# Optimization experiments

Hardware: AMD Instinct MI355X
Metric: run time of the kernel (lower is better)

## Reference

```python
import jax, jax.numpy as jnp
import numpy as np

B, S, F = 8, 4096, 512
H, A, L, DK = 8, 512, 64, 33  # n_head, n_attn, n_landmarks, d_kernel
D = A // H  # d_k = 64


def setup_inputs() -> dict:
    key = jax.random.key(0)
    ks = jax.random.split(key, 12)
    s = 0.02
    return {
        "query": jax.random.normal(ks[0], (B, S, F), jnp.float32),
        "key": jax.random.normal(ks[1], (B, S, F), jnp.float32),
        "value": jax.random.normal(ks[2], (B, S, F), jnp.float32),
        "mask": jnp.ones((B, 1, S), jnp.bool_),
        "Wq": jax.random.normal(ks[3], (F, A), jnp.float32) * s,
        "bq": jnp.zeros((A,), jnp.float32),
        "Wk": jax.random.normal(ks[4], (F, A), jnp.float32) * s,
        "bk": jnp.zeros((A,), jnp.float32),
        "Wv": jax.random.normal(ks[5], (F, A), jnp.float32) * s,
        "bv": jnp.zeros((A,), jnp.float32),
        "Wo": jax.random.normal(ks[6], (A, F), jnp.float32) * s,
        "bo": jnp.zeros((F,), jnp.float32),
        "conv_w": jax.random.normal(ks[7], (H, 1, DK, 1), jnp.float32) * s,
    }


def iterative_inv(mat, n_iter=6):
    # mat: [B, H, L, L]
    I = jnp.eye(mat.shape[-1], dtype=mat.dtype)
    K = mat
    denom = jnp.max(jnp.sum(K, axis=-2), axis=-1)[:, :, None, None]
    V = jnp.swapaxes(K, -1, -2) / denom
    for _ in range(n_iter):
        KV = K @ V
        V = 0.25 * V @ (13 * I - KV @ (15 * I - KV @ (7 * I - KV)))
    return V


def reference(query, key, value, mask, Wq, bq, Wk, bk, Wv, bv, Wo, bo, conv_w):
    nb, seq, _ = query.shape
    q = (query @ Wq + bq).reshape(nb, seq, H, D).transpose(0, 2, 1, 3)  # [B,H,S,D]
    k = (key @ Wk + bk).reshape(nb, seq, H, D).transpose(0, 2, 1, 3)
    v = (value @ Wv + bv).reshape(nb, seq, H, D).transpose(0, 2, 1, 3)
    scale = D ** -0.25
    q = q * scale
    k = k * scale
    m = seq // L + 1  # segment length per landmark
    q_rep = jnp.concatenate([q, q, q], axis=2)[:, :, : m * L, :]
    k_rep = jnp.concatenate([k, k, k], axis=2)[:, :, : m * L, :]
    q_land = q_rep.reshape(nb, H, L, m, D).mean(axis=3)  # [B,H,L,D]
    k_land = k_rep.reshape(nb, H, L, m, D).mean(axis=3)
    ker1 = jax.nn.softmax(jnp.einsum("bhsd,bhld->bhsl", q, k_land), axis=-1)
    ker2 = jax.nn.softmax(jnp.einsum("bhld,bhmd->bhlm", q_land, k_land), axis=-1)
    ker3 = jax.nn.softmax(jnp.einsum("bhld,bhsd->bhls", q_land, k), axis=-1)
    x = ker1 @ (iterative_inv(ker2) @ (ker3 @ v))  # [B,H,S,D]
    # depthwise conv over the sequence axis (kernel (DK,1), groups=H)
    pad = DK // 2
    conv_out = jax.lax.conv_general_dilated(
        v, conv_w, window_strides=(1, 1), padding=((pad, pad), (0, 0)),
        feature_group_count=H, dimension_numbers=("NCHW", "OIHW", "NCHW"))
    x = x + conv_out
    x = x.transpose(0, 2, 1, 3).reshape(nb, seq, H * D)
    return x @ Wo + bo
```

## Files before the change

### kernel.cpp

```cpp
#include <hip/hip_runtime.h>
#include <hip/hip_bf16.h>
#include <hip/hip_fp16.h>

#define SEQ 4096
#define NBATCH 8
#define NHEAD 8
#define DKW 33
#define LDP 68

typedef _Float16 f16x8 __attribute__((ext_vector_type(8)));
typedef _Float16 f16x4 __attribute__((ext_vector_type(4)));
typedef float f32x4 __attribute__((ext_vector_type(4)));

__global__ __launch_bounds__(256) void cvt_w_k(const float* __restrict__ W, _Float16* __restrict__ Wt, float scale)
{
  __shared__ float T[64][65];
  int n0 = blockIdx.x * 64, k0 = blockIdx.y * 64;
  int tid = threadIdx.x;
#pragma unroll
  for (int i = 0; i < 16; i++) {
    int e = i * 256 + tid; int r = e >> 6, c = e & 63;
    T[r][c] = W[(size_t)(k0 + r) * 512 + n0 + c];
  }
  __syncthreads();
#pragma unroll
  for (int i = 0; i < 16; i++) {
    int e = i * 256 + tid; int r = e >> 6, c = e & 63;
    Wt[(size_t)(n0 + r) * 512 + k0 + c] = (_Float16)(T[c][r] * scale);
  }
}

template<typename TA, int ABHSD, int OUTL>
__global__ __launch_bounds__(256) void gemm_f16_k(
    const TA* __restrict__ A, const _Float16* __restrict__ Wt,
    const float* __restrict__ bias, float bscale, void* __restrict__ outp)
{
  __shared__ _Float16 Al[2][128 * 40];
  __shared__ _Float16 Bl[2][128 * 40];
  const int tid = threadIdx.x;
  const int lane = tid & 63, wave = tid >> 6;
  const int wr = wave >> 1, wc = wave & 1;
  const int row0 = blockIdx.x * 128, col0 = blockIdx.y * 128;
  const int ar = tid >> 2;
  const int ak = (tid & 3) * 8;
  const int grA0 = row0 + ar, grA1 = row0 + ar + 64;
  size_t bsA0, bsA1;
  if constexpr (ABHSD) {
    bsA0 = ((size_t)(grA0 >> 12) * NHEAD * SEQ + (grA0 & 4095)) * 64;
    bsA1 = ((size_t)(grA1 >> 12) * NHEAD * SEQ + (grA1 & 4095)) * 64;
  } else {
    bsA0 = (size_t)grA0 * 512;
    bsA1 = (size_t)grA1 * 512;
  }
  const size_t bsB0 = (size_t)(col0 + ar) * 512, bsB1 = (size_t)(col0 + ar + 64) * 512;
  const int lA0 = ar * 40 + ak, lA1 = (ar + 64) * 40 + ak;

  f32x4 acc[4][4];
#pragma unroll
  for (int m = 0; m < 4; m++)
#pragma unroll
    for (int n = 0; n < 4; n++) acc[m][n] = (f32x4){0.f, 0.f, 0.f, 0.f};

  auto loadA = [&](size_t base, int k) -> f16x8 {
    if constexpr (ABHSD) {
      return *(const f16x8*)&A[base + (size_t)(k >> 6) * (SEQ * 64) + (k & 63)];
    } else if constexpr (sizeof(TA) == 4) {
      float4 x = *(const float4*)&A[base + k];
      float4 y = *(const float4*)&A[base + k + 4];
      f16x8 o;
      o[0] = (_Float16)x.x; o[1] = (_Float16)x.y; o[2] = (_Float16)x.z; o[3] = (_Float16)x.w;
      o[4] = (_Float16)y.x; o[5] = (_Float16)y.y; o[6] = (_Float16)y.z; o[7] = (_Float16)y.w;
      return o;
    } else {
      return *(const f16x8*)&A[base + k];
    }
  };

  f16x8 sA0 = loadA(bsA0, ak), sA1 = loadA(bsA1, ak);
  f16x8 sB0 = *(const f16x8*)&Wt[bsB0 + ak];
  f16x8 sB1 = *(const f16x8*)&Wt[bsB1 + ak];
  *(f16x8*)&Al[0][lA0] = sA0;
  *(f16x8*)&Al[0][lA1] = sA1;
  *(f16x8*)&Bl[0][lA0] = sB0;
  *(f16x8*)&Bl[0][lA1] = sB1;
  {
    int k = 32 + ak;
    sA0 = loadA(bsA0, k); sA1 = loadA(bsA1, k);
    sB0 = *(const f16x8*)&Wt[bsB0 + k];
    sB1 = *(const f16x8*)&Wt[bsB1 + k];
  }
  __syncthreads();

  for (int ks = 0; ks < 16; ks++) {
    const int cur = ks & 1;
    f16x8 af[4], bf[4];
#pragma unroll
    for (int m = 0; m < 4; m++)
      af[m] = *(const f16x8*)&Al[cur][(wr * 64 + m * 16 + (lane & 15)) * 40 + (lane >> 4) * 8];
#pragma unroll
    for (int n = 0; n < 4; n++)
      bf[n] = *(const f16x8*)&Bl[cur][(wc * 64 + n * 16 + (lane & 15)) * 40 + (lane >> 4) * 8];
#pragma unroll
    for (int m = 0; m < 4; m++)
#pragma unroll
      for (int n = 0; n < 4; n++)
        acc[m][n] = __builtin_amdgcn_mfma_f32_16x16x32_f16(af[m], bf[n], acc[m][n], 0, 0, 0);
    if (ks < 15) {
      const int nxt = cur ^ 1;
      *(f16x8*)&Al[nxt][lA0] = sA0;
      *(f16x8*)&Al[nxt][lA1] = sA1;
      *(f16x8*)&Bl[nxt][lA0] = sB0;
      *(f16x8*)&Bl[nxt][lA1] = sB1;
      if (ks < 14) {
        int k = (ks + 2) * 32 + ak;
        sA0 = loadA(bsA0, k); sA1 = loadA(bsA1, k);
        sB0 = *(const f16x8*)&Wt[bsB0 + k];
        sB1 = *(const f16x8*)&Wt[bsB1 + k];
      }
    }
    __syncthreads();
  }
  float bb[4];
#pragma unroll
  for (int n = 0; n < 4; n++)
    bb[n] = bias[col0 + wc * 64 + n * 16 + (lane & 15)] * bscale;
#pragma unroll
  for (int m = 0; m < 4; m++) {
    int row_b = row0 + wr * 64 + m * 16 + ((lane >> 4) * 4);
#pragma unroll
    for (int n = 0; n < 4; n++) {
      int col = col0 + wc * 64 + n * 16 + (lane & 15);
#pragma unroll
      for (int r = 0; r < 4; r++) {
        int row = row_b + r;
        float vvv = acc[m][n][r] + bb[n];
        if constexpr (OUTL == 1) {
          int b = row >> 12, s = row & 4095;
          int h = col >> 6, d = col & 63;
          ((_Float16*)outp)[((size_t)(b * NHEAD + h) * SEQ + s) * 64 + d] = (_Float16)vvv;
        } else if constexpr (OUTL == 2) {
          int b = row >> 12, s = row & 4095;
          int h = col >> 6, d = col & 63;
          ((_Float16*)outp)[((size_t)(b * NHEAD + h) * 64 + d) * SEQ + s] = (_Float16)vvv;
        } else {
          ((float*)outp)[(size_t)row * 512 + col] = vvv;
        }
      }
    }
  }
}

__global__ void landmarks_k(const _Float16* __restrict__ q, const _Float16* __restrict__ k,
                            float* __restrict__ qlandf, float* __restrict__ klandf,
                            _Float16* __restrict__ ql16, _Float16* __restrict__ kl16)
{
  int bhl = blockIdx.x;
  int d = threadIdx.x;
  int l = bhl & 63, bh = bhl >> 6;
  const _Float16* qp = q + (size_t)bh * SEQ * 64;
  const _Float16* kp = k + (size_t)bh * SEQ * 64;
  float sq = 0.f, sk = 0.f;
  int base = l * 65;
  for (int i = 0; i < 65; i++) {
    int s = (base + i) & 4095;
    sq += (float)qp[(size_t)s * 64 + d];
    sk += (float)kp[(size_t)s * 64 + d];
  }
  float mq = sq * (1.0f / 65.0f), mk = sk * (1.0f / 65.0f);
  qlandf[(size_t)bhl * 64 + d] = mq;
  klandf[(size_t)bhl * 64 + d] = mk;
  ql16[(size_t)bhl * 64 + d] = (_Float16)mq;
  kl16[(size_t)bhl * 64 + d] = (_Float16)mk;
}

__device__ __forceinline__ void mfma64(
    float (&C)[64][LDP], const float (&X)[64][LDP], const float (&Yt)[64][LDP],
    int wv, int l15, int l4)
{
  f16x8 ah[2], al[2];
#pragma unroll
  for (int kh = 0; kh < 2; kh++) {
    const float* xp = &X[wv * 16 + l15][kh * 32 + l4 * 8];
    float4 x0 = *(const float4*)xp;
    float4 x1 = *(const float4*)(xp + 4);
    float xv[8] = {x0.x, x0.y, x0.z, x0.w, x1.x, x1.y, x1.z, x1.w};
#pragma unroll
    for (int j = 0; j < 8; j++) {
      _Float16 h = (_Float16)xv[j];
      ah[kh][j] = h;
      al[kh][j] = (_Float16)(xv[j] - (float)h);
    }
  }
  f32x4 acc[4];
#pragma unroll
  for (int n = 0; n < 4; n++) {
    f16x8 bh_[2], bl_[2];
#pragma unroll
    for (int kh = 0; kh < 2; kh++) {
      const float* yp = &Yt[n * 16 + l15][kh * 32 + l4 * 8];
      float4 y0 = *(const float4*)yp;
      float4 y1 = *(const float4*)(yp + 4);
      float yv[8] = {y0.x, y0.y, y0.z, y0.w, y1.x, y1.y, y1.z, y1.w};
#pragma unroll
      for (int j = 0; j < 8; j++) {
        _Float16 h = (_Float16)yv[j];
        bh_[kh][j] = h;
        bl_[kh][j] = (_Float16)(yv[j] - (float)h);
      }
    }
    acc[n] = (f32x4){0.f, 0.f, 0.f, 0.f};
#pragma unroll
    for (int kh = 0; kh < 2; kh++) {
      acc[n] = __builtin_amdgcn_mfma_f32_16x16x32_f16(ah[kh], bh_[kh], acc[n], 0, 0, 0);
      acc[n] = __builtin_amdgcn_mfma_f32_16x16x32_f16(ah[kh], bl_[kh], acc[n], 0, 0, 0);
      acc[n] = __builtin_amdgcn_mfma_f32_16x16x32_f16(al[kh], bh_[kh], acc[n], 0, 0, 0);
    }
  }
#pragma unroll
  for (int n = 0; n < 4; n++)
#pragma unroll
    for (int r = 0; r < 4; r++)
      C[wv * 16 + l4 * 4 + r][n * 16 + l15] = acc[n][r];
  __syncthreads();
}

__global__ __launch_bounds__(256) void ker2_inv_k(
    const float* __restrict__ qland, const float* __restrict__ kland, float* __restrict__ invm)
{
  __shared__ float Km[64][LDP], Vm[64][LDP], VmT[64][LDP], KV[64][LDP], T1t[64][LDP], T2[64][LDP];
  __shared__ float colsum[64];
  __shared__ float denom_s;
  int bh = blockIdx.x, tid = threadIdx.x;
  int lane = tid & 63, wv = tid >> 6, l15 = lane & 15, l4 = lane >> 4;
  const float* qlp = qland + (size_t)bh * 4096;
  const float* klp = kland + (size_t)bh * 4096;
  const int r = tid >> 2, cq = (tid & 3) * 16;
#pragma unroll
  for (int j = 0; j < 4; j++) {
    *(float4*)&T2[r][cq + j * 4]  = *(const float4*)&qlp[(size_t)r * 64 + cq + j * 4];
    *(float4*)&T1t[r][cq + j * 4] = *(const float4*)&klp[(size_t)r * 64 + cq + j * 4];
  }
  __syncthreads();
  mfma64(Km, T2, T1t, wv, l15, l4);
  {
    float4 v[4];
#pragma unroll
    for (int j = 0; j < 4; j++) v[j] = *(const float4*)&Km[r][cq + j * 4];
    float mx = -1e30f;
#pragma unroll
    for (int j = 0; j < 4; j++) mx = fmaxf(mx, fmaxf(fmaxf(v[j].x, v[j].y), fmaxf(v[j].z, v[j].w)));
    mx = fmaxf(mx, __shfl_xor(mx, 1));
    mx = fmaxf(mx, __shfl_xor(mx, 2));
    float s = 0.f;
#pragma unroll
    for (int j = 0; j < 4; j++) {
      v[j].x = __expf(v[j].x - mx); v[j].y = __expf(v[j].y - mx);
      v[j].z = __expf(v[j].z - mx); v[j].w = __expf(v[j].w - mx);
      s += v[j].x + v[j].y + v[j].z + v[j].w;
    }
    s += __shfl_xor(s, 1);
    s += __shfl_xor(s, 2);
    float iv = 1.0f / s;
#pragma unroll
    for (int j = 0; j < 4; j++) {
      v[j].x *= iv; v[j].y *= iv; v[j].z *= iv; v[j].w *= iv;
      *(float4*)&Km[r][cq + j * 4] = v[j];
    }
  }
  __syncthreads();
  {
    float s = 0.f;
#pragma unroll
    for (int i = 0; i < 16; i++) s += Km[cq + i][r];
    s += __shfl_xor(s, 1);
    s += __shfl_xor(s, 2);
    if ((tid & 3) == 0) colsum[r] = s;
  }
  __syncthreads();
  if (tid < 64) {
    float v = colsum[tid];
#pragma unroll
    for (int off = 1; off < 64; off <<= 1) v = fmaxf(v, __shfl_xor(v, off));
    if (tid == 0) denom_s = v;
  }
  __syncthreads();
  {
    float dn = 1.0f / denom_s;
#pragma unroll
    for (int j = 0; j < 4; j++) {
      float4 v = *(const float4*)&Km[r][cq + j * 4];
      v.x *= dn; v.y *= dn; v.z *= dn; v.w *= dn;
      *(float4*)&VmT[r][cq + j * 4] = v;
      Vm[cq + j * 4 + 0][r] = v.x;
      Vm[cq + j * 4 + 1][r] = v.y;
      Vm[cq + j * 4 + 2][r] = v.z;
      Vm[cq + j * 4 + 3][r] = v.w;
    }
  }
  __syncthreads();
  for (int it = 0; it < 6; it++) {
    mfma64(KV, Km, VmT, wv, l15, l4);
#pragma unroll
    for (int j = 0; j < 4; j++) {
      float4 v = *(const float4*)&KV[r][cq + j * 4];
#pragma unroll
      for (int e = 0; e < 4; e++) {
        int col = cq + j * 4 + e;
        T1t[col][r] = (r == col ? 7.0f : 0.0f) - ((const float*)&v)[e];
      }
    }
    __syncthreads();
    mfma64(T2, KV, T1t, wv, l15, l4);
#pragma unroll
    for (int j = 0; j < 4; j++) {
      float4 v = *(const float4*)&T2[r][cq + j * 4];
#pragma unroll
      for (int e = 0; e < 4; e++) {
        int col = cq + j * 4 + e;
        T1t[col][r] = (r == col ? 15.0f : 0.0f) - ((const float*)&v)[e];
      }
    }
    __syncthreads();
    mfma64(T2, KV, T1t, wv, l15, l4);
#pragma unroll
    for (int j = 0; j < 4; j++) {
      float4 v = *(const float4*)&T2[r][cq + j * 4];
#pragma unroll
      for (int e = 0; e < 4; e++) {
        int col = cq + j * 4 + e;
        T1t[col][r] = (r == col ? 13.0f : 0.0f) - ((const float*)&v)[e];
      }
    }
    __syncthreads();
    mfma64(T2, Vm, T1t, wv, l15, l4);
#pragma unroll
    for (int j = 0; j < 4; j++) {
      float4 v = *(const float4*)&T2[r][cq + j * 4];
      v.x *= 0.25f; v.y *= 0.25f; v.z *= 0.25f; v.w *= 0.25f;
      *(float4*)&Vm[r][cq + j * 4] = v;
      VmT[cq + j * 4 + 0][r] = v.x;
      VmT[cq + j * 4 + 1][r] = v.y;
      VmT[cq + j * 4 + 2][r] = v.z;
      VmT[cq + j * 4 + 3][r] = v.w;
    }
    __syncthreads();
  }
#pragma unroll
  for (int j = 0; j < 4; j++)
    *(float4*)&invm[(size_t)bh * 4096 + (size_t)r * 64 + cq + j * 4] = *(const float4*)&Vm[r][cq + j * 4];
}

__global__ __launch_bounds__(256) void ker3pv_k(
    const _Float16* __restrict__ kx, const _Float16* __restrict__ vt,
    const _Float16* __restrict__ ql16,
    float* __restrict__ t1part, float* __restrict__ csumpart)
{
  __shared__ __attribute__((aligned(16))) _Float16 kls[64 * 72];
  __shared__ __attribute__((aligned(16))) _Float16 vls[64 * 72];
  __shared__ __attribute__((aligned(16))) _Float16 pls[64 * 72];
  __shared__ float red[4][64];
  int g = blockIdx.x, bh = blockIdx.y;
  int tid = threadIdx.x, lane = tid & 63, wv = tid >> 6;
  const _Float16* kp = kx + (size_t)bh * SEQ * 64;
  const _Float16* vp = vt + (size_t)bh * 64 * SEQ;
  const _Float16* qlp = ql16 + (size_t)bh * 4096;
  const int l15 = lane & 15, l4 = lane >> 4;

  f16x8 qa[4][2];
#pragma unroll
  for (int lt = 0; lt < 4; lt++)
#pragma unroll
    for (int kh = 0; kh < 2; kh++)
      qa[lt][kh] = *(const f16x8*)&qlp[(size_t)(lt * 16 + l15) * 64 + kh * 32 + l4 * 8];

  float cs[16];
#pragma unroll
  for (int i = 0; i < 16; i++) cs[i] = 0.f;
  f32x4 accp[4];
#pragma unroll
  for (int lt = 0; lt < 4; lt++) accp[lt] = (f32x4){0.f, 0.f, 0.f, 0.f};

  const int srow = tid >> 2, c4 = tid & 3;
  for (int t = 0; t < 16; t++) {
    int s0 = g * 1024 + t * 64;
    __syncthreads();
    *(f16x8*)&kls[srow * 72 + c4 * 8]       = *(const f16x8*)&kp[(size_t)(s0 + srow) * 64 + c4 * 8];
    *(f16x8*)&kls[srow * 72 + (c4 + 4) * 8] = *(const f16x8*)&kp[(size_t)(s0 + srow) * 64 + (c4 + 4) * 8];
    *(f16x8*)&vls[srow * 72 + c4 * 8]       = *(const f16x8*)&vp[(size_t)srow * SEQ + s0 + c4 * 8];
    *(f16x8*)&vls[srow * 72 + (c4 + 4) * 8] = *(const f16x8*)&vp[(size_t)srow * SEQ + s0 + (c4 + 4) * 8];
    __syncthreads();
    f16x8 kb[2];
    kb[0] = *(const f16x8*)&kls[(wv * 16 + l15) * 72 + l4 * 8];
    kb[1] = *(const f16x8*)&kls[(wv * 16 + l15) * 72 + 32 + l4 * 8];
    f32x4 C[4];
#pragma unroll
    for (int lt = 0; lt < 4; lt++) {
      C[lt] = (f32x4){0.f, 0.f, 0.f, 0.f};
      C[lt] = __builtin_amdgcn_mfma_f32_16x16x32_f16(qa[lt][0], kb[0], C[lt], 0, 0, 0);
      C[lt] = __builtin_amdgcn_mfma_f32_16x16x32_f16(qa[lt][1], kb[1], C[lt], 0, 0, 0);
    }
#pragma unroll
    for (int lt = 0; lt < 4; lt++)
#pragma unroll
      for (int r = 0; r < 4; r++) {
        float e = __expf(C[lt][r]);
        cs[lt * 4 + r] += e;
        pls[(lt * 16 + l4 * 4 + r) * 72 + wv * 16 + l15] = (_Float16)e;
      }
    __syncthreads();
    f16x8 va[2];
    va[0] = *(const f16x8*)&vls[(wv * 16 + l15) * 72 + l4 * 8];
    va[1] = *(const f16x8*)&vls[(wv * 16 + l15) * 72 + 32 + l4 * 8];
#pragma unroll
    for (int lt = 0; lt < 4; lt++) {
      f16x8 pb0 = *(const f16x8*)&pls[(lt * 16 + l15) * 72 + l4 * 8];
      f16x8 pb1 = *(const f16x8*)&pls[(lt * 16 + l15) * 72 + 32 + l4 * 8];
      accp[lt] = __builtin_amdgcn_mfma_f32_16x16x32_f16(va[0], pb0, accp[lt], 0, 0, 0);
      accp[lt] = __builtin_amdgcn_mfma_f32_16x16x32_f16(va[1], pb1, accp[lt], 0, 0, 0);
    }
  }
  size_t pbase = ((size_t)(bh * 4 + g)) * 4096;
#pragma unroll
  for (int lt = 0; lt < 4; lt++)
#pragma unroll
    for (int r = 0; r < 4; r++)
      t1part[pbase + (size_t)(wv * 16 + l4 * 4 + r) * 64 + lt * 16 + l15] = accp[lt][r];
#pragma unroll
  for (int i = 0; i < 16; i++) {
    cs[i] += __shfl_xor(cs[i], 1);
    cs[i] += __shfl_xor(cs[i], 2);
    cs[i] += __shfl_xor(cs[i], 4);
    cs[i] += __shfl_xor(cs[i], 8);
  }
  if (l15 == 0) {
#pragma unroll
    for (int lt = 0; lt < 4; lt++)
#pragma unroll
      for (int r = 0; r < 4; r++)
        red[wv][lt * 16 + l4 * 4 + r] = cs[lt * 4 + r];
  }
  __syncthreads();
  if (tid < 64)
    csumpart[((size_t)(bh * 4 + g)) * 64 + tid] = red[0][tid] + red[1][tid] + red[2][tid] + red[3][tid];
}

__global__ void t1_reduce_k(const float* __restrict__ t1part, const float* __restrict__ csumpart,
                            float* __restrict__ t1r)
{
  int i = blockIdx.x * 256 + threadIdx.x;
  int bh = i >> 12, dl = i & 4095, l = dl & 63;
  float s = 0.f, cssum = 0.f;
#pragma unroll
  for (int g = 0; g < 4; g++) {
    s += t1part[(((size_t)(bh * 4 + g)) << 12) + dl];
    cssum += csumpart[(((size_t)(bh * 4 + g)) << 6) + l];
  }
  t1r[i] = s / cssum;
}

__global__ __launch_bounds__(256) void t2_mm_k(
    const float* __restrict__ invm, const float* __restrict__ t1r, _Float16* __restrict__ t2t)
{
  __shared__ float T[64][68];
  __shared__ float I[64][68];
  int bh = blockIdx.x;
  int tid = threadIdx.x;
  const float* ip = invm + (size_t)bh * 4096;
  const float* tp = t1r + (size_t)bh * 4096;
  int r = tid >> 2;
#pragma unroll
  for (int mq = 0; mq < 4; mq++) {
    int d0 = (tid & 3) * 16 + mq * 4;
    *(float4*)&T[r][d0] = *(const float4*)&tp[(size_t)r * 64 + d0];
    *(float4*)&I[r][d0] = *(const float4*)&ip[(size_t)r * 64 + d0];
  }
  __syncthreads();
  int ty = tid >> 4, tx = tid & 15;
  float acc[4][4] = {};
#pragma unroll 4
  for (int kk = 0; kk < 64; kk++) {
    float a_[4], b_[4];
#pragma unroll
    for (int i = 0; i < 4; i++) a_[i] = T[ty * 4 + i][kk];
#pragma unroll
    for (int j = 0; j < 4; j++) b_[j] = I[tx * 4 + j][kk];
#pragma unroll
    for (int i = 0; i < 4; i++)
#pragma unroll
      for (int j = 0; j < 4; j++)
        acc[i][j] = fmaf(a_[i], b_[j], acc[i][j]);
  }
#pragma unroll
  for (int i = 0; i < 4; i++) {
    f16x4 o;
    o[0] = (_Float16)acc[i][0]; o[1] = (_Float16)acc[i][1];
    o[2] = (_Float16)acc[i][2]; o[3] = (_Float16)acc[i][3];
    *(f16x4*)&t2t[(size_t)bh * 4096 + (size_t)(ty * 4 + i) * 64 + tx * 4] = o;
  }
}

__global__ __launch_bounds__(256) void x1_k(
    const _Float16* __restrict__ qx, const _Float16* __restrict__ kl16,
    const _Float16* __restrict__ t2t, _Float16* __restrict__ xq)
{
  __shared__ __attribute__((aligned(16))) _Float16 qls[64 * 72];
  __shared__ __attribute__((aligned(16))) _Float16 t2ls[64 * 72];
  __shared__ __attribute__((aligned(16))) _Float16 pls[64 * 72];
  int c = blockIdx.x, bh = blockIdx.y;
  int s0 = c * 64;
  int tid = threadIdx.x, lane = tid & 63, wv = tid >> 6;
  const int l15 = lane & 15, l4 = lane >> 4;
  const _Float16* qp = qx + ((size_t)bh * SEQ + s0) * 64;
  const int srow = tid >> 2, c4 = tid & 3;
  *(f16x8*)&qls[srow * 72 + c4 * 8]       = *(const f16x8*)&qp[(size_t)srow * 64 + c4 * 8];
  *(f16x8*)&qls[srow * 72 + (c4 + 4) * 8] = *(const f16x8*)&qp[(size_t)srow * 64 + (c4 + 4) * 8];
  *(f16x8*)&t2ls[srow * 72 + c4 * 8]       = *(const f16x8*)&t2t[(size_t)bh * 4096 + (size_t)srow * 64 + c4 * 8];
  *(f16x8*)&t2ls[srow * 72 + (c4 + 4) * 8] = *(const f16x8*)&t2t[(size_t)bh * 4096 + (size_t)srow * 64 + (c4 + 4) * 8];
  f16x8 klb[4][2];
#pragma unroll
  for (int lt = 0; lt < 4; lt++)
#pragma unroll
    for (int kh = 0; kh < 2; kh++)
      klb[lt][kh] = *(const f16x8*)&kl16[(size_t)bh * 4096 + (size_t)(lt * 16 + l15) * 64 + kh * 32 + l4 * 8];
  __syncthreads();
  f16x8 qaf[2];
  qaf[0] = *(const f16x8*)&qls[(wv * 16 + l15) * 72 + l4 * 8];
  qaf[1] = *(const f16x8*)&qls[(wv * 16 + l15) * 72 + 32 + l4 * 8];
  f32x4 C[4];
#pragma unroll
  for (int lt = 0; lt < 4; lt++) {
    C[lt] = (f32x4){0.f, 0.f, 0.f, 0.f};
    C[lt] = __builtin_amdgcn_mfma_f32_16x16x32_f16(qaf[0], klb[lt][0], C[lt], 0, 0, 0);
    C[lt] = __builtin_amdgcn_mfma_f32_16x16x32_f16(qaf[1], klb[lt][1], C[lt], 0, 0, 0);
  }
  float e[16], rs[4];
#pragma unroll
  for (int r = 0; r < 4; r++) rs[r] = 0.f;
#pragma unroll
  for (int lt = 0; lt < 4; lt++)
#pragma unroll
    for (int r = 0; r < 4; r++) {
      e[lt * 4 + r] = __expf(C[lt][r]);
      rs[r] += e[lt * 4 + r];
    }
#pragma unroll
  for (int r = 0; r < 4; r++) {
    rs[r] += __shfl_xor(rs[r], 1);
    rs[r] += __shfl_xor(rs[r], 2);
    rs[r] += __shfl_xor(rs[r], 4);
    rs[r] += __shfl_xor(rs[r], 8);
    rs[r] = 1.0f / rs[r];
  }
#pragma unroll
  for (int lt = 0; lt < 4; lt++)
#pragma unroll
    for (int r = 0; r < 4; r++)
      pls[(wv * 16 + l4 * 4 + r) * 72 + lt * 16 + l15] = (_Float16)(e[lt * 4 + r] * rs[r]);
  __syncthreads();
  f16x8 pa[2];
  pa[0] = *(const f16x8*)&pls[(wv * 16 + l15) * 72 + l4 * 8];
  pa[1] = *(const f16x8*)&pls[(wv * 16 + l15) * 72 + 32 + l4 * 8];
#pragma unroll
  for (int dt = 0; dt < 4; dt++) {
    f16x8 tb0 = *(const f16x8*)&t2ls[(dt * 16 + l15) * 72 + l4 * 8];
    f16x8 tb1 = *(const f16x8*)&t2ls[(dt * 16 + l15) * 72 + 32 + l4 * 8];
    f32x4 X = (f32x4){0.f, 0.f, 0.f, 0.f};
    X = __builtin_amdgcn_mfma_f32_16x16x32_f16(pa[0], tb0, X, 0, 0, 0);
    X = __builtin_amdgcn_mfma_f32_16x16x32_f16(pa[1], tb1, X, 0, 0, 0);
#pragma unroll
    for (int r = 0; r < 4; r++) {
      int s = s0 + wv * 16 + l4 * 4 + r;
      int d = dt * 16 + l15;
      xq[((size_t)bh * SEQ + s) * 64 + d] = (_Float16)X[r];
    }
  }
}

__global__ __launch_bounds__(256) void conv_add_k(
    const _Float16* __restrict__ vt, const float* __restrict__ cw, _Float16* __restrict__ xq)
{
  __shared__ _Float16 vls[64 * 98];
  __shared__ _Float16 ct[64 * 72];
  int c = blockIdx.x, bh = blockIdx.y;
  int h = bh & 7;
  int tid = threadIdx.x;
  int sc = c * 64;
  {
    int row = tid >> 2, seg = tid & 3;
    const _Float16* vp = vt + ((size_t)bh * 64 + row) * SEQ;
    int base = sc - 16 + seg * 24;
#pragma unroll
    for (int i = 0; i < 3; i++) {
      int s = base + i * 8;
      f16x8 v;
      if (s >= 0 && s + 8 <= SEQ) {
        v = *(const f16x8*)&vp[s];
      } else {
#pragma unroll
        for (int j = 0; j < 8; j++) {
          int sj = s + j;
          v[j] = (sj >= 0 && sj < SEQ) ? vp[sj] : (_Float16)0.f;
        }
      }
      *(f16x8*)&vls[row * 98 + seg * 24 + i * 8] = v;
    }
  }
  float w[DKW];
#pragma unroll
  for (int j = 0; j < DKW; j++) w[j] = cw[h * DKW + j];
  __syncthreads();
  {
    int d = tid & 63, sg = tid >> 6;
    float win[48];
#pragma unroll
    for (int t = 0; t < 48; t++) win[t] = (float)vls[d * 98 + sg * 16 + t];
#pragma unroll
    for (int i = 0; i < 16; i++) {
      float acc = 0.f;
#pragma unroll
      for (int j = 0; j < DKW; j++) acc = fmaf(w[j], win[i + j], acc);
      ct[(sg * 16 + i) * 72 + d] = (_Float16)acc;
    }
  }
  __syncthreads();
#pragma unroll
  for (int it = 0; it < 2; it++) {
    int e = it * 256 + tid;
    int s = e >> 3, d0 = (e & 7) * 8;
    size_t gi = ((size_t)bh * SEQ + sc + s) * 64 + d0;
    f16x8 x = *(const f16x8*)&xq[gi];
    f16x8 cc = *(const f16x8*)&ct[s * 72 + d0];
#pragma unroll
    for (int j = 0; j < 8; j++) x[j] = (_Float16)((float)x[j] + (float)cc[j]);
    *(f16x8*)&xq[gi] = x;
  }
}

extern "C" void kernel_launch(void* const* d_in, const int* in_sizes, int n_in,
                              void* d_out, int out_size, void* d_ws, size_t ws_size,
                              hipStream_t stream)
{
  (void)in_sizes; (void)n_in; (void)out_size; (void)ws_size;
  const float* query = (const float*)d_in[0];
  const float* key_  = (const float*)d_in[1];
  const float* value = (const float*)d_in[2];
  const float* Wq = (const float*)d_in[4];
  const float* bq = (const float*)d_in[5];
  const float* Wk = (const float*)d_in[6];
  const float* bk = (const float*)d_in[7];
  const float* Wv = (const float*)d_in[8];
  const float* bv = (const float*)d_in[9];
  const float* Wo = (const float*)d_in[10];
  const float* bo = (const float*)d_in[11];
  const float* cw = (const float*)d_in[12];
  float* out = (float*)d_out;

  const size_t NQ = (size_t)NBATCH * NHEAD * SEQ * 64;
  _Float16* qh  = (_Float16*)d_ws;
  _Float16* kh  = qh + NQ;
  _Float16* vt  = kh + NQ;
  _Float16* WqT = vt + NQ;
  _Float16* WkT = WqT + 262144;
  _Float16* WvT = WkT + 262144;
  _Float16* WoT = WvT + 262144;
  _Float16* ql16 = WoT + 262144;
  _Float16* kl16 = ql16 + 262144;
  _Float16* t2t  = kl16 + 262144;
  float* qlandf = (float*)(t2t + 262144);
  float* klandf = qlandf + 262144;
  float* invb   = klandf + 262144;
  float* t1r    = invb + 262144;
  float* t1part = t1r + 262144;
  float* csumpart = t1part + 4 * 262144;

  const float scl = 0.3535533905932738f;

  cvt_w_k<<<dim3(8, 8), 256, 0, stream>>>(Wq, WqT, scl);
  cvt_w_k<<<dim3(8, 8), 256, 0, stream>>>(Wk, WkT, scl);
  cvt_w_k<<<dim3(8, 8), 256, 0, stream>>>(Wv, WvT, 1.0f);
  cvt_w_k<<<dim3(8, 8), 256, 0, stream>>>(Wo, WoT, 1.0f);

  dim3 gg(256, 4);
  gemm_f16_k<float, 0, 1><<<gg, 256, 0, stream>>>(query, WqT, bq, scl, qh);
  gemm_f16_k<float, 0, 1><<<gg, 256, 0, stream>>>(key_,  WkT, bk, scl, kh);
  gemm_f16_k<float, 0, 2><<<gg, 256, 0, stream>>>(value, WvT, bv, 1.0f, vt);

  landmarks_k<<<4096, 64, 0, stream>>>(qh, kh, qlandf, klandf, ql16, kl16);
  ker2_inv_k<<<64, 256, 0, stream>>>(qlandf, klandf, invb);
  ker3pv_k<<<dim3(4, 64), 256, 0, stream>>>(kh, vt, ql16, t1part, csumpart);
  t1_reduce_k<<<1024, 256, 0, stream>>>(t1part, csumpart, t1r);
  t2_mm_k<<<64, 256, 0, stream>>>(invb, t1r, t2t);
  x1_k<<<dim3(64, 64), 256, 0, stream>>>(qh, kl16, t2t, qh);
  conv_add_k<<<dim3(64, 64), 256, 0, stream>>>(vt, cw, qh);
  gemm_f16_k<_Float16, 1, 0><<<gg, 256, 0, stream>>>(qh, WoT, bo, 1.0f, out);
}
```

Before: 325.8 us.

## Keep full weight panel in LDS and stream A fragments directly from global

Replaces the double-buffered 128x128 GEMM with a 512x128 tile per block. The whole 128x512 weight slice is held in LDS once, and each wave loads its A fragments straight from global memory into registers with one-step prefetch, so the K-loop has no per-step barriers. The transposed V output is staged through LDS for coalesced 16-byte stores along the sequence axis. The cost is about 130KB of LDS per block and a large accumulator set, which limits occupancy, and the A fragment loads from global are uncoalesced.

Result: no change. 324.3 us (-0.4%).

```diff
diff --git a/kernel.cpp b/kernel.cpp
--- a/kernel.cpp
+++ b/kernel.cpp
@@ -31,119 +31,128 @@
 }
 
 template<typename TA, int ABHSD, int OUTL>
-__global__ __launch_bounds__(256) void gemm_f16_k(
+__global__ __launch_bounds__(512, 2) void gemm_bp_k(
     const TA* __restrict__ A, const _Float16* __restrict__ Wt,
     const float* __restrict__ bias, float bscale, void* __restrict__ outp)
 {
-  __shared__ _Float16 Al[2][128 * 40];
-  __shared__ _Float16 Bl[2][128 * 40];
+  __shared__ __attribute__((aligned(16))) _Float16 Bl[128 * 516];
   const int tid = threadIdx.x;
-  const int lane = tid & 63, wave = tid >> 6;
-  const int wr = wave >> 1, wc = wave & 1;
-  const int row0 = blockIdx.x * 128, col0 = blockIdx.y * 128;
-  const int ar = tid >> 2;
-  const int ak = (tid & 3) * 8;
-  const int grA0 = row0 + ar, grA1 = row0 + ar + 64;
-  size_t bsA0, bsA1;
-  if constexpr (ABHSD) {
-    bsA0 = ((size_t)(grA0 >> 12) * NHEAD * SEQ + (grA0 & 4095)) * 64;
-    bsA1 = ((size_t)(grA1 >> 12) * NHEAD * SEQ + (grA1 & 4095)) * 64;
-  } else {
-    bsA0 = (size_t)grA0 * 512;
-    bsA1 = (size_t)grA1 * 512;
-  }
-  const size_t bsB0 = (size_t)(col0 + ar) * 512, bsB1 = (size_t)(col0 + ar + 64) * 512;
-  const int lA0 = ar * 40 + ak, lA1 = (ar + 64) * 40 + ak;
-
-  f32x4 acc[4][4];
-#pragma unroll
-  for (int m = 0; m < 4; m++)
-#pragma unroll
-    for (int n = 0; n < 4; n++) acc[m][n] = (f32x4){0.f, 0.f, 0.f, 0.f};
-
-  auto loadA = [&](size_t base, int k) -> f16x8 {
+  const int lane = tid & 63, wv = tid >> 6;
+  const int l15 = lane & 15, l4 = lane >> 4;
+  const int col0 = blockIdx.y * 128;
+  const int row0 = blockIdx.x * 512;
+
+  {
+    int n = tid >> 2, kc = (tid & 3) * 128;
+    const _Float16* wp = &Wt[(size_t)(col0 + n) * 512 + kc];
+    _Float16* lp = &Bl[n * 516 + kc];
+#pragma unroll
+    for (int i = 0; i < 16; i++)
+      *(f16x8*)&lp[i * 8] = *(const f16x8*)&wp[i * 8];
+  }
+
+  size_t abase[4];
+#pragma unroll
+  for (int mt = 0; mt < 4; mt++) {
+    int grow = row0 + wv * 64 + mt * 16 + l15;
+    if constexpr (ABHSD)
+      abase[mt] = ((size_t)(grow >> 12) * (NHEAD * SEQ) + (grow & 4095)) * 64;
+    else
+      abase[mt] = (size_t)grow * 512;
+  }
+
+  auto loadA = [&](int mt, int ks) -> f16x8 {
+    int k = ks * 32 + l4 * 8;
     if constexpr (ABHSD) {
-      return *(const f16x8*)&A[base + (size_t)(k >> 6) * (SEQ * 64) + (k & 63)];
+      return *(const f16x8*)&A[abase[mt] + (size_t)(k >> 6) * (SEQ * 64) + (k & 63)];
     } else if constexpr (sizeof(TA) == 4) {
-      float4 x = *(const float4*)&A[base + k];
-      float4 y = *(const float4*)&A[base + k + 4];
+      float4 x = *(const float4*)&A[abase[mt] + k];
+      float4 y = *(const float4*)&A[abase[mt] + k + 4];
       f16x8 o;
       o[0] = (_Float16)x.x; o[1] = (_Float16)x.y; o[2] = (_Float16)x.z; o[3] = (_Float16)x.w;
       o[4] = (_Float16)y.x; o[5] = (_Float16)y.y; o[6] = (_Float16)y.z; o[7] = (_Float16)y.w;
       return o;
     } else {
-      return *(const f16x8*)&A[base + k];
+      return *(const f16x8*)&A[abase[mt] + k];
     }
   };
 
-  f16x8 sA0 = loadA(bsA0, ak), sA1 = loadA(bsA1, ak);
-  f16x8 sB0 = *(const f16x8*)&Wt[bsB0 + ak];
-  f16x8 sB1 = *(const f16x8*)&Wt[bsB1 + ak];
-  *(f16x8*)&Al[0][lA0] = sA0;
-  *(f16x8*)&Al[0][lA1] = sA1;
-  *(f16x8*)&Bl[0][lA0] = sB0;
-  *(f16x8*)&Bl[0][lA1] = sB1;
-  {
-    int k = 32 + ak;
-    sA0 = loadA(bsA0, k); sA1 = loadA(bsA1, k);
-    sB0 = *(const f16x8*)&Wt[bsB0 + k];
-    sB1 = *(const f16x8*)&Wt[bsB1 + k];
-  }
+  f32x4 acc[4][8];
+#pragma unroll
+  for (int mt = 0; mt < 4; mt++)
+#pragma unroll
+    for (int n = 0; n < 8; n++) acc[mt][n] = (f32x4){0.f, 0.f, 0.f, 0.f};
+
+  f16x8 aC[4];
+#pragma unroll
+  for (int mt = 0; mt < 4; mt++) aC[mt] = loadA(mt, 0);
   __syncthreads();
 
   for (int ks = 0; ks < 16; ks++) {
-    const int cur = ks & 1;
-    f16x8 af[4], bf[4];
-#pragma unroll
-    for (int m = 0; m < 4; m++)
-      af[m] = *(const f16x8*)&Al[cur][(wr * 64 + m * 16 + (lane & 15)) * 40 + (lane >> 4) * 8];
-#pragma unroll
-    for (int n = 0; n < 4; n++)
-      bf[n] = *(const f16x8*)&Bl[cur][(wc * 64 + n * 16 + (lane & 15)) * 40 + (lane >> 4) * 8];
-#pragma unroll
-    for (int m = 0; m < 4; m++)
-#pragma unroll
-      for (int n = 0; n < 4; n++)
-        acc[m][n] = __builtin_amdgcn_mfma_f32_16x16x32_f16(af[m], bf[n], acc[m][n], 0, 0, 0);
+    f16x8 aN[4];
     if (ks < 15) {
-      const int nxt = cur ^ 1;
-      *(f16x8*)&Al[nxt][lA0] = sA0;
-      *(f16x8*)&Al[nxt][lA1] = sA1;
-      *(f16x8*)&Bl[nxt][lA0] = sB0;
-      *(f16x8*)&Bl[nxt][lA1] = sB1;
-      if (ks < 14) {
-        int k = (ks + 2) * 32 + ak;
-        sA0 = loadA(bsA0, k); sA1 = loadA(bsA1, k);
-        sB0 = *(const f16x8*)&Wt[bsB0 + k];
-        sB1 = *(const f16x8*)&Wt[bsB1 + k];
+#pragma unroll
+      for (int mt = 0; mt < 4; mt++) aN[mt] = loadA(mt, ks + 1);
+    }
+    f16x8 bf[8];
+#pragma unroll
+    for (int n = 0; n < 8; n++)
+      bf[n] = *(const f16x8*)&Bl[(n * 16 + l15) * 516 + ks * 32 + l4 * 8];
+#pragma unroll
+    for (int mt = 0; mt < 4; mt++)
+#pragma unroll
+      for (int n = 0; n < 8; n++)
+        acc[mt][n] = __builtin_amdgcn_mfma_f32_16x16x32_f16(aC[mt], bf[n], acc[mt][n], 0, 0, 0);
+    if (ks < 15) {
+#pragma unroll
+      for (int mt = 0; mt < 4; mt++) aC[mt] = aN[mt];
+    }
+  }
+
+  float bb[8];
+#pragma unroll
+  for (int n = 0; n < 8; n++) bb[n] = bias[col0 + n * 16 + l15] * bscale;
+
+  if constexpr (OUTL == 2) {
+    __syncthreads();
+#pragma unroll
+    for (int mt = 0; mt < 4; mt++)
+#pragma unroll
+      for (int n = 0; n < 8; n++) {
+        f16x4 o;
+#pragma unroll
+        for (int r = 0; r < 4; r++) o[r] = (_Float16)(acc[mt][n][r] + bb[n]);
+        *(f16x4*)&Bl[(n * 16 + l15) * 516 + wv * 64 + mt * 16 + l4 * 4] = o;
       }
-    }
-    __syncthreads();
-  }
-  float bb[4];
-#pragma unroll
-  for (int n = 0; n < 4; n++)
-    bb[n] = bias[col0 + wc * 64 + n * 16 + (lane & 15)] * bscale;
-#pragma unroll
-  for (int m = 0; m < 4; m++) {
-    int row_b = row0 + wr * 64 + m * 16 + ((lane >> 4) * 4);
-#pragma unroll
-    for (int n = 0; n < 4; n++) {
-      int col = col0 + wc * 64 + n * 16 + (lane & 15);
-#pragma unroll
-      for (int r = 0; r < 4; r++) {
-        int row = row_b + r;
-        float vvv = acc[m][n][r] + bb[n];
-        if constexpr (OUTL == 1) {
-          int b = row >> 12, s = row & 4095;
-          int h = col >> 6, d = col & 63;
-          ((_Float16*)outp)[((size_t)(b * NHEAD + h) * SEQ + s) * 64 + d] = (_Float16)vvv;
-        } else if constexpr (OUTL == 2) {
-          int b = row >> 12, s = row & 4095;
-          int h = col >> 6, d = col & 63;
-          ((_Float16*)outp)[((size_t)(b * NHEAD + h) * 64 + d) * SEQ + s] = (_Float16)vvv;
-        } else {
-          ((float*)outp)[(size_t)row * 512 + col] = vvv;
+    __syncthreads();
+    int b = row0 >> 12, sbase = row0 & 4095;
+#pragma unroll
+    for (int i = 0; i < 16; i++) {
+      int idx = i * 512 + tid;
+      int c = idx >> 6, sc = (idx & 63) * 8;
+      int colg = col0 + c;
+      int h = colg >> 6, d = colg & 63;
+      f16x8 v = *(const f16x8*)&Bl[c * 516 + sc];
+      *(f16x8*)&((_Float16*)outp)[((size_t)((b * NHEAD + h) * 64 + d)) * SEQ + sbase + sc] = v;
+    }
+  } else {
+#pragma unroll
+    for (int mt = 0; mt < 4; mt++) {
+      int rb = row0 + wv * 64 + mt * 16 + l4 * 4;
+#pragma unroll
+      for (int n = 0; n < 8; n++) {
+        int col = col0 + n * 16 + l15;
+#pragma unroll
+        for (int r = 0; r < 4; r++) {
+          int row = rb + r;
+          float vv = acc[mt][n][r] + bb[n];
+          if constexpr (OUTL == 1) {
+            int b = row >> 12, s = row & 4095;
+            int h = col >> 6, d = col & 63;
+            ((_Float16*)outp)[((size_t)(b * NHEAD + h) * SEQ + s) * 64 + d] = (_Float16)vv;
+          } else {
+            ((float*)outp)[(size_t)row * 512 + col] = vv;
+          }
         }
       }
     }
@@ -680,10 +689,10 @@
   cvt_w_k<<<dim3(8, 8), 256, 0, stream>>>(Wv, WvT, 1.0f);
   cvt_w_k<<<dim3(8, 8), 256, 0, stream>>>(Wo, WoT, 1.0f);
 
-  dim3 gg(256, 4);
-  gemm_f16_k<float, 0, 1><<<gg, 256, 0, stream>>>(query, WqT, bq, scl, qh);
-  gemm_f16_k<float, 0, 1><<<gg, 256, 0, stream>>>(key_,  WkT, bk, scl, kh);
-  gemm_f16_k<float, 0, 2><<<gg, 256, 0, stream>>>(value, WvT, bv, 1.0f, vt);
+  dim3 gg(64, 4);
+  gemm_bp_k<float, 0, 1><<<gg, 512, 0, stream>>>(query, WqT, bq, scl, qh);
+  gemm_bp_k<float, 0, 1><<<gg, 512, 0, stream>>>(key_,  WkT, bk, scl, kh);
+  gemm_bp_k<float, 0, 2><<<gg, 512, 0, stream>>>(value, WvT, bv, 1.0f, vt);
 
   landmarks_k<<<4096, 64, 0, stream>>>(qh, kh, qlandf, klandf, ql16, kl16);
   ker2_inv_k<<<64, 256, 0, stream>>>(qlandf, klandf, invb);
@@ -692,5 +701,5 @@
   t2_mm_k<<<64, 256, 0, stream>>>(invb, t1r, t2t);
   x1_k<<<dim3(64, 64), 256, 0, stream>>>(qh, kl16, t2t, qh);
   conv_add_k<<<dim3(64, 64), 256, 0, stream>>>(vt, cw, qh);
-  gemm_f16_k<_Float16, 1, 0><<<gg, 256, 0, stream>>>(qh, WoT, bo, 1.0f, out);
-}
+  gemm_bp_k<_Float16, 1, 0><<<gg, 512, 0, stream>>>(qh, WoT, bo, 1.0f, out);
+}
```
